# Performance work log

Hardware: AMD Instinct MI355X
Metric: run time of the kernel (lower is better)

Reference implementation:

```python
import jax, jax.numpy as jnp
import numpy as np

L = 3          # num_layer
E_DIM = 64     # emb_dim
B = 4          # graphs per batch
N = 20000      # nodes per graph
E = 320000     # edges per graph
IN_DIM = 21    # raw node feature dim (Linear(21, emb_dim))
BN_EPS = 1e-5


def setup_inputs() -> dict:
    key = jax.random.key(0)
    ks = jax.random.split(key, 16)
    h2 = 2 * E_DIM
    inp = {
        "x": jax.random.normal(ks[0], (B, N, IN_DIM), dtype=jnp.float32),
        "edge_index": jax.random.randint(ks[1], (B, 2, E), 0, N, dtype=jnp.int64),
        "edge_attr": jax.random.normal(ks[2], (B, E, 1), dtype=jnp.float32),
        # layer-0 input node embedding Linear(21, emb)
        "inW": jax.random.normal(ks[3], (IN_DIM, E_DIM), dtype=jnp.float32) * 0.1,
        "inb": jnp.zeros((E_DIM,), dtype=jnp.float32),
        # per-layer edge encoder Linear(1, emb)
        "edgeW": jax.random.normal(ks[4], (L, 1, E_DIM), dtype=jnp.float32) * 0.1,
        "edgeb": jnp.zeros((L, E_DIM), dtype=jnp.float32),
        # per-layer MLP: Linear(2e,2e) -> BN(2e) -> ReLU -> Linear(2e,e)
        "W1": jax.random.normal(ks[5], (L, h2, h2), dtype=jnp.float32) * 0.05,
        "b1": jnp.zeros((L, h2), dtype=jnp.float32),
        "gamma": jnp.ones((L, h2), dtype=jnp.float32),
        "beta": jnp.zeros((L, h2), dtype=jnp.float32),
        "W2": jax.random.normal(ks[6], (L, h2, E_DIM), dtype=jnp.float32) * 0.05,
        "b2": jnp.zeros((L, E_DIM), dtype=jnp.float32),
    }
    return inp


def _batchnorm_train(h, g, b):
    # BatchNorm1d in training mode: per-graph stats over the node dim, biased var
    m = h.mean(axis=0)
    v = jnp.mean((h - m) ** 2, axis=0)
    return (h - m) * jax.lax.rsqrt(v + BN_EPS) * g + b


def _gin_layer(xg, eig, eag, W1l, b1l, gl, bel, W2l, b2l):
    # xg [N,e], eig [2,E], eag [E,e]
    x_j = xg[eig[0]]                                   # gather source nodes [E,e]
    msg = jnp.concatenate([x_j, eag], axis=-1)         # [E,2e]
    aggr = jax.ops.segment_sum(msg, eig[1], num_segments=N)  # scatter-add [N,2e]
    h = aggr @ W1l + b1l
    h = _batchnorm_train(h, gl, bel)
    h = jax.nn.relu(h)
    return h @ W2l + b2l                               # [N,e]


def reference(x, edge_index, edge_attr, inW, inb, edgeW, edgeb, W1, b1, gamma, beta, W2, b2):
    h = x
    for l in range(L):
        ea = edge_attr @ edgeW[l] + edgeb[l]           # [B,E,e] edge embeddings
        if l == 0:
            h = h @ inW + inb                          # [B,N,e]
        h = jax.vmap(_gin_layer, in_axes=(0, 0, 0, None, None, None, None, None, None))(
            h, edge_index, ea, W1[l], b1[l], gamma[l], beta[l], W2[l], b2[l])
        if l < L - 1:                                  # drop_ratio=0 -> dropout is identity
            h = jax.nn.relu(h)
    return h  # JK='last'
```

## Files before the change

kernel.cpp:

```cpp
#include <hip/hip_runtime.h>
#include <hip/hip_bf16.h>
#include <hip/hip_fp16.h>

#define NB 4
#define NN 20000
#define NE 320000
#define IND 21
#define ED 64
#define H2 128
#define CAP 48
#define RNODES 2500
#define ECHUNK 2560
#define BN_EPS 1e-5f

typedef __attribute__((ext_vector_type(8))) short bf16x8;
typedef __attribute__((ext_vector_type(4))) float f32x4;

__device__ __forceinline__ short f2bf(float f) {
    unsigned u = __float_as_uint(f);
    u += 0x7fffu + ((u >> 16) & 1u);
    return (short)(u >> 16);
}


__global__ __launch_bounds__(256) void k_fill_direct(
    const int* __restrict__ ei, const float* __restrict__ eattr,
    int* __restrict__ cnt, unsigned int* __restrict__ bucket)
{
    const int b = blockIdx.y;
    const int range = blockIdx.x & 7;
    const int chunk = blockIdx.x >> 3;
    const int lo = range * RNODES, hi = lo + RNODES;
    const int* srcp = ei + (size_t)b * 2 * NE;
    const int* dstp = srcp + NE;
    const float* ap = eattr + (size_t)b * NE;
    #pragma unroll
    for (int it = 0; it < ECHUNK / 256; ++it) {
        const int e = chunk * ECHUNK + it * 256 + threadIdx.x;
        const int dst = dstp[e];
        if (dst >= lo && dst < hi) {
            const int src = srcp[e];
            const float a = ap[e];
            const int node = b * NN + dst;
            const int p = atomicAdd(&cnt[node], 1);
            if (p < CAP)
                bucket[(size_t)node * CAP + p] =
                    ((unsigned int)src & 0xffffu) | (__float_as_uint(a) & 0xffff0000u);
        }
    }
}

__global__ __launch_bounds__(256) void k_in(
    const float* __restrict__ x, const float* __restrict__ inW,
    const float* __restrict__ inb, __half* __restrict__ h)
{
    const int b = blockIdx.y;
    const int t = blockIdx.x * 256 + threadIdx.x;
    const int n = t >> 6;
    const int c = t & 63;
    if (n >= NN) return;
    const float* xr = x + ((size_t)b * NN + n) * IND;
    float acc = inb[c];
    #pragma unroll
    for (int k = 0; k < IND; ++k) acc += xr[k] * inW[k * ED + c];
    h[((size_t)b * NN + n) * ED + c] = __float2half(acc);
}

__global__ __launch_bounds__(256) void k_prep(
    const float* __restrict__ W1, const float* __restrict__ W2,
    const float* __restrict__ edgeW, const float* __restrict__ edgeb,
    short* __restrict__ W1T, short* __restrict__ W2T,
    float* __restrict__ uv_all, float* __restrict__ stats_all)
{
    const int l = blockIdx.x;
    const int tid = threadIdx.x;
    ((float4*)(stats_all + l * 1024))[tid] = make_float4(0.f, 0.f, 0.f, 0.f);
    for (int i = tid; i < H2 * ED; i += 256) {
        const int j = i >> 6, k = i & 63;
        W1T[l * 8192 + i] = f2bf(W1[(size_t)l * H2 * H2 + k * H2 + j]);
    }
    for (int i = tid; i < ED * H2; i += 256) {
        const int c = i >> 7, k = i & 127;
        W2T[l * 8192 + i] = f2bf(W2[(size_t)l * H2 * ED + k * ED + c]);
    }
    if (tid < H2) {
        float u = 0.f, v = 0.f;
        for (int k = 0; k < ED; ++k) {
            const float w = W1[(size_t)l * H2 * H2 + (ED + k) * H2 + tid];
            u += edgeW[l * ED + k] * w;
            v += edgeb[l * ED + k] * w;
        }
        uv_all[l * 256 + tid] = u;
        uv_all[l * 256 + H2 + tid] = v;
    }
}


__global__ __launch_bounds__(256) void k_aggr_stats(
    const __half* __restrict__ h, const unsigned int* __restrict__ bucket,
    const int* __restrict__ cnt_arr, const short* __restrict__ W1Tl,
    const float* __restrict__ b1l, const float* __restrict__ uv_l,
    short* __restrict__ aggr_bf, float* __restrict__ s_attr,
    float* __restrict__ stats_l, int write_sattr)
{
    __shared__ short w1t[H2 * 72];
    __shared__ short atb[16 * 72];
    __shared__ float sdl[16], ddl[16];
    __shared__ float uL[H2], vL[H2], bbL[H2];
    const int tid = threadIdx.x;
    const int g = blockIdx.x & 7;
    const int b = g >> 1;
    const int t = ((int)blockIdx.x >> 3) * 2 + (g & 1);
    const int n0 = t * 16;

    for (int i = tid; i < 1024; i += 256)
        *(uint4*)&w1t[(i >> 3) * 72 + (i & 7) * 8] = ((const uint4*)W1Tl)[i];
    if (tid < H2) { uL[tid] = uv_l[tid]; vL[tid] = uv_l[H2 + tid]; bbL[tid] = b1l[tid]; }

    {
        const int node = n0 + (tid >> 4);
        const int q = tid & 15;
        const int cntraw = cnt_arr[b * NN + node];
        const int cnt = min(cntraw, CAP);
        const unsigned int* row = bucket + (size_t)(b * NN + node) * CAP;
        const __half* hp = h + (size_t)b * NN * ED + q * 4;
        float4 a0 = make_float4(0.f, 0.f, 0.f, 0.f);
        float4 a1 = make_float4(0.f, 0.f, 0.f, 0.f);
        float sa = 0.f;
        int j = 0;
        for (; j + 4 <= cnt; j += 4) {
            const uint4 ss = *(const uint4*)(row + j);
            const uint2 r0 = *(const uint2*)(hp + (size_t)(ss.x & 0xffffu) * ED);
            const uint2 r1 = *(const uint2*)(hp + (size_t)(ss.y & 0xffffu) * ED);
            const uint2 r2 = *(const uint2*)(hp + (size_t)(ss.z & 0xffffu) * ED);
            const uint2 r3 = *(const uint2*)(hp + (size_t)(ss.w & 0xffffu) * ED);
            sa += __uint_as_float(ss.x & 0xffff0000u) + __uint_as_float(ss.y & 0xffff0000u)
                + __uint_as_float(ss.z & 0xffff0000u) + __uint_as_float(ss.w & 0xffff0000u);
            const float2 f0a = __half22float2(*(const __half2*)&r0.x);
            const float2 f0b = __half22float2(*(const __half2*)&r0.y);
            const float2 f1a = __half22float2(*(const __half2*)&r1.x);
            const float2 f1b = __half22float2(*(const __half2*)&r1.y);
            const float2 f2a = __half22float2(*(const __half2*)&r2.x);
            const float2 f2b = __half22float2(*(const __half2*)&r2.y);
            const float2 f3a = __half22float2(*(const __half2*)&r3.x);
            const float2 f3b = __half22float2(*(const __half2*)&r3.y);
            a0.x += f0a.x + f1a.x; a0.y += f0a.y + f1a.y;
            a0.z += f0b.x + f1b.x; a0.w += f0b.y + f1b.y;
            a1.x += f2a.x + f3a.x; a1.y += f2a.y + f3a.y;
            a1.z += f2b.x + f3b.x; a1.w += f2b.y + f3b.y;
        }
        for (; j < cnt; ++j) {
            const unsigned e = row[j];
            sa += __uint_as_float(e & 0xffff0000u);
            const uint2 r0 = *(const uint2*)(hp + (size_t)(e & 0xffffu) * ED);
            const float2 fa = __half22float2(*(const __half2*)&r0.x);
            const float2 fb = __half22float2(*(const __half2*)&r0.y);
            a0.x += fa.x; a0.y += fa.y; a0.z += fb.x; a0.w += fb.y;
        }
        a0.x += a1.x; a0.y += a1.y; a0.z += a1.z; a0.w += a1.w;
        uint2 pk;
        pk.x = (unsigned short)f2bf(a0.x) | ((unsigned int)(unsigned short)f2bf(a0.y) << 16);
        pk.y = (unsigned short)f2bf(a0.z) | ((unsigned int)(unsigned short)f2bf(a0.w) << 16);
        *(uint2*)&atb[(tid >> 4) * 72 + q * 4] = pk;
        *(uint2*)&aggr_bf[((size_t)b * NN + node) * ED + q * 4] = pk;
        if (q == 0) {
            sdl[tid >> 4] = sa;
            ddl[tid >> 4] = (float)cntraw;
            if (write_sattr) s_attr[b * NN + node] = sa;
        }
    }
    __syncthreads();

    const int l = tid & 63;
    const int w = tid >> 6;
    const int m = l & 15, quad = l >> 4;
    f32x4 acc0 = {0.f, 0.f, 0.f, 0.f}, acc1 = {0.f, 0.f, 0.f, 0.f};
    #pragma unroll
    for (int kc = 0; kc < 2; ++kc) {
        const bf16x8 fa = *(const bf16x8*)&atb[m * 72 + kc * 32 + quad * 8];
        const bf16x8 fb0 = *(const bf16x8*)&w1t[((w * 2 + 0) * 16 + m) * 72 + kc * 32 + quad * 8];
        const bf16x8 fb1 = *(const bf16x8*)&w1t[((w * 2 + 1) * 16 + m) * 72 + kc * 32 + quad * 8];
        acc0 = __builtin_amdgcn_mfma_f32_16x16x32_bf16(fa, fb0, acc0, 0, 0, 0);
        acc1 = __builtin_amdgcn_mfma_f32_16x16x32_bf16(fa, fb1, acc1, 0, 0, 0);
    }
    float sa_r[4], dg_r[4];
    #pragma unroll
    for (int r = 0; r < 4; ++r) { sa_r[r] = sdl[quad * 4 + r]; dg_r[r] = ddl[quad * 4 + r]; }
    #pragma unroll
    for (int t2 = 0; t2 < 2; ++t2) {
        const int j = (w * 2 + t2) * 16 + m;
        const float u = uL[j], v = vL[j], bb = bbL[j];
        float ls = 0.f, lq = 0.f;
        #pragma unroll
        for (int r = 0; r < 4; ++r) {
            const float h1 = (t2 ? acc1[r] : acc0[r]) + sa_r[r] * u + dg_r[r] * v + bb;
            ls += h1; lq += h1 * h1;
        }
        ls += __shfl_xor(ls, 16); ls += __shfl_xor(ls, 32);
        lq += __shfl_xor(lq, 16); lq += __shfl_xor(lq, 32);
        if (l < 16) {
            atomicAdd(&stats_l[b * H2 + j], ls);
            atomicAdd(&stats_l[NB * H2 + b * H2 + j], lq);
        }
    }
}

__global__ __launch_bounds__(256) void k_mlp_out(
    const short* __restrict__ aggr_bf, const float* __restrict__ s_attr,
    const int* __restrict__ cnt_arr, const short* __restrict__ W1Tl,
    const short* __restrict__ W2Tl, const float* __restrict__ b1l,
    const float* __restrict__ uv_l, const float* __restrict__ stats_l,
    const float* __restrict__ gamma_l, const float* __restrict__ beta_l,
    const float* __restrict__ b2l, __half* __restrict__ outh,
    float* __restrict__ outf, int last)
{
    __shared__ short wt[H2 * 72];
    __shared__ short ab[32 * 72];
    __shared__ short pb[32 * 136];
    __shared__ float sdl[32], ddl[32];
    __shared__ float uL[H2], vL[H2], bbL[H2], scL[H2], shL[H2];
    const int tid = threadIdx.x;
    const int g = blockIdx.x & 7;
    const int b = g >> 1;
    const int t = ((int)blockIdx.x >> 3) * 2 + (g & 1);
    if (t >= NN / 32) return;
    const int n0 = t * 32;

    for (int i = tid; i < 1024; i += 256)
        *(uint4*)&wt[(i >> 3) * 72 + (i & 7) * 8] = ((const uint4*)W1Tl)[i];
    *(uint4*)&ab[(tid >> 3) * 72 + (tid & 7) * 8] =
        ((const uint4*)(aggr_bf + ((size_t)b * NN + n0) * ED))[tid];
    if (tid < 32) sdl[tid] = s_attr[b * NN + n0 + tid];
    else if (tid < 64) ddl[tid - 32] = (float)cnt_arr[b * NN + n0 + tid - 32];
    if (tid < H2) {
        const int j = tid;
        const float mm = stats_l[b * H2 + j] * (1.f / NN);
        const float var = fmaxf(stats_l[NB * H2 + b * H2 + j] * (1.f / NN) - mm * mm, 0.f);
        const float rs = rsqrtf(var + BN_EPS);
        const float sc = gamma_l[j] * rs;
        scL[j] = sc;
        shL[j] = beta_l[j] - mm * sc;
        uL[j] = uv_l[j]; vL[j] = uv_l[H2 + j]; bbL[j] = b1l[j];
    }
    __syncthreads();

    const int l = tid & 63;
    const int w = tid >> 6;
    const int m = l & 15, quad = l >> 4;
    const int mt = w & 1;
    {
        const int jb = (w >> 1) * 4;
        f32x4 acc[4];
        #pragma unroll
        for (int i = 0; i < 4; ++i) acc[i] = (f32x4){0.f, 0.f, 0.f, 0.f};
        #pragma unroll
        for (int kc = 0; kc < 2; ++kc) {
            const bf16x8 fa = *(const bf16x8*)&ab[(mt * 16 + m) * 72 + kc * 32 + quad * 8];
            #pragma unroll
            for (int t2 = 0; t2 < 4; ++t2) {
                const bf16x8 fb = *(const bf16x8*)&wt[((jb + t2) * 16 + m) * 72 + kc * 32 + quad * 8];
                acc[t2] = __builtin_amdgcn_mfma_f32_16x16x32_bf16(fa, fb, acc[t2], 0, 0, 0);
            }
        }
        float sa_r[4], dg_r[4];
        #pragma unroll
        for (int r = 0; r < 4; ++r) {
            const int row = mt * 16 + quad * 4 + r;
            sa_r[r] = sdl[row]; dg_r[r] = ddl[row];
        }
        #pragma unroll
        for (int t2 = 0; t2 < 4; ++t2) {
            const int j = (jb + t2) * 16 + m;
            const float u = uL[j], v = vL[j], bb = bbL[j];
            const float sc = scL[j], sh = shL[j];
            #pragma unroll
            for (int r = 0; r < 4; ++r) {
                const float h1 = acc[t2][r] + sa_r[r] * u + dg_r[r] * v + bb;
                pb[(mt * 16 + quad * 4 + r) * 136 + j] = f2bf(fmaxf(h1 * sc + sh, 0.f));
            }
        }
    }
    __syncthreads();
    for (int i = tid; i < 1024; i += 256)
        *(uint4*)&wt[(i >> 4) * 136 + (i & 15) * 8] = ((const uint4*)W2Tl)[i];
    __syncthreads();
    {
        const int nb = (w >> 1) * 2;
        f32x4 acc2[2];
        acc2[0] = (f32x4){0.f, 0.f, 0.f, 0.f};
        acc2[1] = (f32x4){0.f, 0.f, 0.f, 0.f};
        #pragma unroll
        for (int kc = 0; kc < 4; ++kc) {
            const bf16x8 fa = *(const bf16x8*)&pb[(mt * 16 + m) * 136 + kc * 32 + quad * 8];
            #pragma unroll
            for (int t2 = 0; t2 < 2; ++t2) {
                const bf16x8 fb = *(const bf16x8*)&wt[((nb + t2) * 16 + m) * 136 + kc * 32 + quad * 8];
                acc2[t2] = __builtin_amdgcn_mfma_f32_16x16x32_bf16(fa, fb, acc2[t2], 0, 0, 0);
            }
        }
        #pragma unroll
        for (int t2 = 0; t2 < 2; ++t2) {
            const int c = (nb + t2) * 16 + m;
            const float bb2 = b2l[c];
            #pragma unroll
            for (int r = 0; r < 4; ++r) {
                const int row = mt * 16 + quad * 4 + r;
                const size_t idx = ((size_t)b * NN + n0 + row) * ED + c;
                float o = acc2[t2][r] + bb2;
                if (last) outf[idx] = o;
                else outh[idx] = __float2half(fmaxf(o, 0.f));
            }
        }
    }
}


extern "C" void kernel_launch(void* const* d_in, const int* in_sizes, int n_in,
                              void* d_out, int out_size, void* d_ws, size_t ws_size,
                              hipStream_t stream) {
    const float* x     = (const float*)d_in[0];
    const int*   ei    = (const int*)d_in[1];
    const float* eattr = (const float*)d_in[2];
    const float* inW   = (const float*)d_in[3];
    const float* inb   = (const float*)d_in[4];
    const float* edgeW = (const float*)d_in[5];
    const float* edgeb = (const float*)d_in[6];
    const float* W1    = (const float*)d_in[7];
    const float* b1    = (const float*)d_in[8];
    const float* gamma = (const float*)d_in[9];
    const float* beta  = (const float*)d_in[10];
    const float* W2    = (const float*)d_in[11];
    const float* b2    = (const float*)d_in[12];
    float* out = (float*)d_out;

    float* s_attr = (float*)d_ws;
    int*   cnt    = (int*)(s_attr + NB * NN);
    unsigned int* bucket = (unsigned int*)(cnt + NB * NN);
    short* aggr_bf = (short*)(bucket + (size_t)NB * NN * CAP);
    __half* hh    = (__half*)(aggr_bf + (size_t)NB * NN * ED);
    short* W1T    = (short*)(hh + (size_t)NB * NN * ED);
    short* W2T    = W1T + 3 * 8192;
    float* uv_all = (float*)(W2T + 3 * 8192);
    float* stats  = uv_all + 3 * 256;

    hipMemsetAsync(cnt, 0, (size_t)NB * NN * sizeof(int), stream);

    const dim3 eg((NE / ECHUNK) * 8, NB);
    k_fill_direct<<<eg, 256, 0, stream>>>(ei, eattr, cnt, bucket);
    k_in<<<dim3(NN * ED / 256, NB), 256, 0, stream>>>(x, inW, inb, hh);
    k_prep<<<3, 256, 0, stream>>>(W1, W2, edgeW, edgeb, W1T, W2T, uv_all, stats);

    const int nblk1 = NB * (NN / 16);
    const int nblk2 = ((NN / 32 + 1) / 2) * 16;
    for (int l = 0; l < 3; ++l) {
        k_aggr_stats<<<nblk1, 256, 0, stream>>>(hh, bucket, cnt,
            W1T + l * 8192, b1 + l * H2, uv_all + l * 256,
            aggr_bf, s_attr, stats + l * 1024, (l == 0) ? 1 : 0);
        k_mlp_out<<<nblk2, 256, 0, stream>>>(aggr_bf, s_attr, cnt,
            W1T + l * 8192, W2T + l * 8192, b1 + l * H2, uv_all + l * 256,
            stats + l * 1024, gamma + l * H2, beta + l * H2, b2 + l * ED,
            hh, out, (l == 2) ? 1 : 0);
    }
}
```

Before: 386.1 us.

## Two-pass edge bucketing and larger node tiles in aggregation and MLP kernels

The direct bucket fill, which had each of 8 node ranges rescan every edge, is replaced by two passes. A compaction pass bins edges by destination range into staging buffers using shared-memory atomics, then a scatter pass fills the per-node buckets. The aggregation kernel now handles 32 nodes per block with 16-byte gathers (8 halves per thread) and 4 MFMA tiles per wave. The MLP kernel handles 64 nodes per block with a bounds check on the ragged last tile. This cuts redundant edge reads and raises per-block work and load width, at the cost of an extra launch and a staging buffer. Staging capacity is fixed, so a skewed edge distribution could overflow it.

```diff
diff --git a/kernel.cpp b/kernel.cpp
--- a/kernel.cpp
+++ b/kernel.cpp
@@ -10,7 +10,7 @@
 #define H2 128
 #define CAP 48
 #define RNODES 2500
-#define ECHUNK 2560
+#define SCAP 45056
 #define BN_EPS 1e-5f
 
 typedef __attribute__((ext_vector_type(8))) short bf16x8;
@@ -22,30 +22,72 @@
     return (short)(u >> 16);
 }
 
-
-__global__ __launch_bounds__(256) void k_fill_direct(
+__device__ __forceinline__ void add8(float* ac, const uint4 rv) {
+    const float2 f0 = __half22float2(*(const __half2*)&rv.x);
+    const float2 f1 = __half22float2(*(const __half2*)&rv.y);
+    const float2 f2 = __half22float2(*(const __half2*)&rv.z);
+    const float2 f3 = __half22float2(*(const __half2*)&rv.w);
+    ac[0] += f0.x; ac[1] += f0.y; ac[2] += f1.x; ac[3] += f1.y;
+    ac[4] += f2.x; ac[5] += f2.y; ac[6] += f3.x; ac[7] += f3.y;
+}
+
+
+__global__ __launch_bounds__(256) void k_compact(
     const int* __restrict__ ei, const float* __restrict__ eattr,
-    int* __restrict__ cnt, unsigned int* __restrict__ bucket)
-{
+    uint2* __restrict__ stage, int* __restrict__ rcnt)
+{
+    __shared__ uint2 bins[8][384];
+    __shared__ int lcnt[8];
+    __shared__ int lbase[8];
     const int b = blockIdx.y;
-    const int range = blockIdx.x & 7;
-    const int chunk = blockIdx.x >> 3;
-    const int lo = range * RNODES, hi = lo + RNODES;
+    const int e0 = blockIdx.x * 2048;
+    const int tid = threadIdx.x;
+    if (tid < 8) lcnt[tid] = 0;
+    __syncthreads();
     const int* srcp = ei + (size_t)b * 2 * NE;
     const int* dstp = srcp + NE;
     const float* ap = eattr + (size_t)b * NE;
     #pragma unroll
-    for (int it = 0; it < ECHUNK / 256; ++it) {
-        const int e = chunk * ECHUNK + it * 256 + threadIdx.x;
-        const int dst = dstp[e];
-        if (dst >= lo && dst < hi) {
+    for (int it = 0; it < 8; ++it) {
+        const int e = e0 + it * 256 + tid;
+        if (e < NE) {
+            const int dst = dstp[e];
             const int src = srcp[e];
             const float a = ap[e];
-            const int node = b * NN + dst;
+            const int r = dst / RNODES;
+            const unsigned lo = ((unsigned)src & 0xffffu) | (__float_as_uint(a) & 0xffff0000u);
+            const int p = atomicAdd(&lcnt[r], 1);
+            if (p < 384) bins[r][p] = make_uint2(lo, (unsigned)dst);
+        }
+    }
+    __syncthreads();
+    if (tid < 8) lbase[tid] = atomicAdd(&rcnt[b * 8 + tid], min(lcnt[tid], 384));
+    __syncthreads();
+    for (int r = 0; r < 8; ++r) {
+        const int c = min(lcnt[r], 384);
+        uint2* dstg = stage + (size_t)(b * 8 + r) * SCAP + lbase[r];
+        for (int i = tid; i < c; i += 256) dstg[i] = bins[r][i];
+    }
+}
+
+__global__ __launch_bounds__(256) void k_scatter(
+    const uint2* __restrict__ stage, const int* __restrict__ rcnt,
+    int* __restrict__ cnt, unsigned int* __restrict__ bucket)
+{
+    const int r = blockIdx.x & 7;
+    const int q = blockIdx.x >> 3;
+    const int b = q & 3;
+    const int slice = q >> 2;
+    const int count = rcnt[b * 8 + r];
+    const uint2* st = stage + (size_t)(b * 8 + r) * SCAP;
+    #pragma unroll
+    for (int it = 0; it < 16; ++it) {
+        const int idx = slice * 4096 + it * 256 + threadIdx.x;
+        if (idx < count) {
+            const uint2 rec = st[idx];
+            const int node = b * NN + (int)rec.y;
             const int p = atomicAdd(&cnt[node], 1);
-            if (p < CAP)
-                bucket[(size_t)node * CAP + p] =
-                    ((unsigned int)src & 0xffffu) | (__float_as_uint(a) & 0xffff0000u);
+            if (p < CAP) bucket[(size_t)node * CAP + p] = rec.x;
         }
     }
 }
@@ -104,68 +146,58 @@
     float* __restrict__ stats_l, int write_sattr)
 {
     __shared__ short w1t[H2 * 72];
-    __shared__ short atb[16 * 72];
-    __shared__ float sdl[16], ddl[16];
+    __shared__ short atb[32 * 72];
+    __shared__ float sdl[32], ddl[32];
     __shared__ float uL[H2], vL[H2], bbL[H2];
     const int tid = threadIdx.x;
     const int g = blockIdx.x & 7;
     const int b = g >> 1;
     const int t = ((int)blockIdx.x >> 3) * 2 + (g & 1);
-    const int n0 = t * 16;
+    if (t >= NN / 32) return;
+    const int n0 = t * 32;
 
     for (int i = tid; i < 1024; i += 256)
         *(uint4*)&w1t[(i >> 3) * 72 + (i & 7) * 8] = ((const uint4*)W1Tl)[i];
     if (tid < H2) { uL[tid] = uv_l[tid]; vL[tid] = uv_l[H2 + tid]; bbL[tid] = b1l[tid]; }
 
     {
-        const int node = n0 + (tid >> 4);
-        const int q = tid & 15;
+        const int node = n0 + (tid >> 3);
+        const int q = tid & 7;
         const int cntraw = cnt_arr[b * NN + node];
         const int cnt = min(cntraw, CAP);
         const unsigned int* row = bucket + (size_t)(b * NN + node) * CAP;
-        const __half* hp = h + (size_t)b * NN * ED + q * 4;
-        float4 a0 = make_float4(0.f, 0.f, 0.f, 0.f);
-        float4 a1 = make_float4(0.f, 0.f, 0.f, 0.f);
+        const __half* hp = h + (size_t)b * NN * ED + q * 8;
+        float ac[8];
+        #pragma unroll
+        for (int i = 0; i < 8; ++i) ac[i] = 0.f;
         float sa = 0.f;
         int j = 0;
         for (; j + 4 <= cnt; j += 4) {
             const uint4 ss = *(const uint4*)(row + j);
-            const uint2 r0 = *(const uint2*)(hp + (size_t)(ss.x & 0xffffu) * ED);
-            const uint2 r1 = *(const uint2*)(hp + (size_t)(ss.y & 0xffffu) * ED);
-            const uint2 r2 = *(const uint2*)(hp + (size_t)(ss.z & 0xffffu) * ED);
-            const uint2 r3 = *(const uint2*)(hp + (size_t)(ss.w & 0xffffu) * ED);
+            const uint4 r0 = *(const uint4*)(hp + (size_t)(ss.x & 0xffffu) * ED);
+            const uint4 r1 = *(const uint4*)(hp + (size_t)(ss.y & 0xffffu) * ED);
+            const uint4 r2 = *(const uint4*)(hp + (size_t)(ss.z & 0xffffu) * ED);
+            const uint4 r3 = *(const uint4*)(hp + (size_t)(ss.w & 0xffffu) * ED);
             sa += __uint_as_float(ss.x & 0xffff0000u) + __uint_as_float(ss.y & 0xffff0000u)
                 + __uint_as_float(ss.z & 0xffff0000u) + __uint_as_float(ss.w & 0xffff0000u);
-            const float2 f0a = __half22float2(*(const __half2*)&r0.x);
-            const float2 f0b = __half22float2(*(const __half2*)&r0.y);
-            const float2 f1a = __half22float2(*(const __half2*)&r1.x);
-            const float2 f1b = __half22float2(*(const __half2*)&r1.y);
-            const float2 f2a = __half22float2(*(const __half2*)&r2.x);
-            const float2 f2b = __half22float2(*(const __half2*)&r2.y);
-            const float2 f3a = __half22float2(*(const __half2*)&r3.x);
-            const float2 f3b = __half22float2(*(const __half2*)&r3.y);
-            a0.x += f0a.x + f1a.x; a0.y += f0a.y + f1a.y;
-            a0.z += f0b.x + f1b.x; a0.w += f0b.y + f1b.y;
-            a1.x += f2a.x + f3a.x; a1.y += f2a.y + f3a.y;
-            a1.z += f2b.x + f3b.x; a1.w += f2b.y + f3b.y;
+            add8(ac, r0); add8(ac, r1); add8(ac, r2); add8(ac, r3);
         }
         for (; j < cnt; ++j) {
             const unsigned e = row[j];
             sa += __uint_as_float(e & 0xffff0000u);
-            const uint2 r0 = *(const uint2*)(hp + (size_t)(e & 0xffffu) * ED);
-            const float2 fa = __half22float2(*(const __half2*)&r0.x);
-            const float2 fb = __half22float2(*(const __half2*)&r0.y);
-            a0.x += fa.x; a0.y += fa.y; a0.z += fb.x; a0.w += fb.y;
-        }
-        a0.x += a1.x; a0.y += a1.y; a0.z += a1.z; a0.w += a1.w;
-        uint2 pk;
-        pk.x = (unsigned short)f2bf(a0.x) | ((unsigned int)(unsigned short)f2bf(a0.y) << 16);
-        pk.y = (unsigned short)f2bf(a0.z) | ((unsigned int)(unsigned short)f2bf(a0.w) << 16);
-        *(uint2*)&atb[(tid >> 4) * 72 + q * 4] = pk;
-        *(uint2*)&aggr_bf[((size_t)b * NN + node) * ED + q * 4] = pk;
+            const uint4 r0 = *(const uint4*)(hp + (size_t)(e & 0xffffu) * ED);
+            add8(ac, r0);
+        }
+        uint4 pk;
+        pk.x = (unsigned short)f2bf(ac[0]) | ((unsigned int)(unsigned short)f2bf(ac[1]) << 16);
+        pk.y = (unsigned short)f2bf(ac[2]) | ((unsigned int)(unsigned short)f2bf(ac[3]) << 16);
+        pk.z = (unsigned short)f2bf(ac[4]) | ((unsigned int)(unsigned short)f2bf(ac[5]) << 16);
+        pk.w = (unsigned short)f2bf(ac[6]) | ((unsigned int)(unsigned short)f2bf(ac[7]) << 16);
+        *(uint4*)&atb[(tid >> 3) * 72 + q * 8] = pk;
+        *(uint4*)&aggr_bf[((size_t)b * NN + node) * ED + q * 8] = pk;
         if (q == 0) {
-            sdl[tid >> 4] = sa;
-            ddl[tid >> 4] = (float)cntraw;
+            sdl[tid >> 3] = sa;
+            ddl[tid >> 3] = (float)cntraw;
             if (write_sattr) s_attr[b * NN + node] = sa;
         }
     }
@@ -174,26 +206,34 @@
     const int l = tid & 63;
     const int w = tid >> 6;
     const int m = l & 15, quad = l >> 4;
-    f32x4 acc0 = {0.f, 0.f, 0.f, 0.f}, acc1 = {0.f, 0.f, 0.f, 0.f};
+    const int mt = w & 1;
+    const int jb = (w >> 1) * 4;
+    f32x4 acc[4];
+    #pragma unroll
+    for (int i = 0; i < 4; ++i) acc[i] = (f32x4){0.f, 0.f, 0.f, 0.f};
     #pragma unroll
     for (int kc = 0; kc < 2; ++kc) {
-        const bf16x8 fa = *(const bf16x8*)&atb[m * 72 + kc * 32 + quad * 8];
-        const bf16x8 fb0 = *(const bf16x8*)&w1t[((w * 2 + 0) * 16 + m) * 72 + kc * 32 + quad * 8];
-        const bf16x8 fb1 = *(const bf16x8*)&w1t[((w * 2 + 1) * 16 + m) * 72 + kc * 32 + quad * 8];
-        acc0 = __builtin_amdgcn_mfma_f32_16x16x32_bf16(fa, fb0, acc0, 0, 0, 0);
-        acc1 = __builtin_amdgcn_mfma_f32_16x16x32_bf16(fa, fb1, acc1, 0, 0, 0);
+        const bf16x8 fa = *(const bf16x8*)&atb[(mt * 16 + m) * 72 + kc * 32 + quad * 8];
+        #pragma unroll
+        for (int t2 = 0; t2 < 4; ++t2) {
+            const bf16x8 fb = *(const bf16x8*)&w1t[((jb + t2) * 16 + m) * 72 + kc * 32 + quad * 8];
+            acc[t2] = __builtin_amdgcn_mfma_f32_16x16x32_bf16(fa, fb, acc[t2], 0, 0, 0);
+        }
     }
     float sa_r[4], dg_r[4];
     #pragma unroll
-    for (int r = 0; r < 4; ++r) { sa_r[r] = sdl[quad * 4 + r]; dg_r[r] = ddl[quad * 4 + r]; }
-    #pragma unroll
-    for (int t2 = 0; t2 < 2; ++t2) {
-        const int j = (w * 2 + t2) * 16 + m;
+    for (int r = 0; r < 4; ++r) {
+        const int row = mt * 16 + quad * 4 + r;
+        sa_r[r] = sdl[row]; dg_r[r] = ddl[row];
+    }
+    #pragma unroll
+    for (int t2 = 0; t2 < 4; ++t2) {
+        const int j = (jb + t2) * 16 + m;
         const float u = uL[j], v = vL[j], bb = bbL[j];
         float ls = 0.f, lq = 0.f;
         #pragma unroll
         for (int r = 0; r < 4; ++r) {
-            const float h1 = (t2 ? acc1[r] : acc0[r]) + sa_r[r] * u + dg_r[r] * v + bb;
+            const float h1 = acc[t2][r] + sa_r[r] * u + dg_r[r] * v + bb;
             ls += h1; lq += h1 * h1;
         }
         ls += __shfl_xor(ls, 16); ls += __shfl_xor(ls, 32);
@@ -215,23 +255,24 @@
     float* __restrict__ outf, int last)
 {
     __shared__ short wt[H2 * 72];
-    __shared__ short ab[32 * 72];
-    __shared__ short pb[32 * 136];
-    __shared__ float sdl[32], ddl[32];
+    __shared__ short ab[64 * 72];
+    __shared__ short pb[64 * 136];
+    __shared__ float sdl[64], ddl[64];
     __shared__ float uL[H2], vL[H2], bbL[H2], scL[H2], shL[H2];
     const int tid = threadIdx.x;
     const int g = blockIdx.x & 7;
     const int b = g >> 1;
     const int t = ((int)blockIdx.x >> 3) * 2 + (g & 1);
-    if (t >= NN / 32) return;
-    const int n0 = t * 32;
+    if (t >= (NN + 63) / 64) return;
+    const int n0 = t * 64;
 
     for (int i = tid; i < 1024; i += 256)
         *(uint4*)&wt[(i >> 3) * 72 + (i & 7) * 8] = ((const uint4*)W1Tl)[i];
-    *(uint4*)&ab[(tid >> 3) * 72 + (tid & 7) * 8] =
-        ((const uint4*)(aggr_bf + ((size_t)b * NN + n0) * ED))[tid];
-    if (tid < 32) sdl[tid] = s_attr[b * NN + n0 + tid];
-    else if (tid < 64) ddl[tid - 32] = (float)cnt_arr[b * NN + n0 + tid - 32];
+    for (int i = tid; i < 512; i += 256)
+        *(uint4*)&ab[(i >> 3) * 72 + (i & 7) * 8] =
+            ((const uint4*)(aggr_bf + ((size_t)b * NN + n0) * ED))[i];
+    if (tid < 64) sdl[tid] = s_attr[b * NN + n0 + tid];
+    else if (tid < 128) ddl[tid - 64] = (float)cnt_arr[b * NN + n0 + tid - 64];
     if (tid < H2) {
         const int j = tid;
         const float mm = stats_l[b * H2 + j] * (1.f / NN);
@@ -247,36 +288,34 @@
     const int l = tid & 63;
     const int w = tid >> 6;
     const int m = l & 15, quad = l >> 4;
-    const int mt = w & 1;
     {
-        const int jb = (w >> 1) * 4;
-        f32x4 acc[4];
-        #pragma unroll
-        for (int i = 0; i < 4; ++i) acc[i] = (f32x4){0.f, 0.f, 0.f, 0.f};
+        f32x4 acc[8];
+        #pragma unroll
+        for (int i = 0; i < 8; ++i) acc[i] = (f32x4){0.f, 0.f, 0.f, 0.f};
         #pragma unroll
         for (int kc = 0; kc < 2; ++kc) {
-            const bf16x8 fa = *(const bf16x8*)&ab[(mt * 16 + m) * 72 + kc * 32 + quad * 8];
+            const bf16x8 fa = *(const bf16x8*)&ab[(w * 16 + m) * 72 + kc * 32 + quad * 8];
             #pragma unroll
-            for (int t2 = 0; t2 < 4; ++t2) {
-                const bf16x8 fb = *(const bf16x8*)&wt[((jb + t2) * 16 + m) * 72 + kc * 32 + quad * 8];
+            for (int t2 = 0; t2 < 8; ++t2) {
+                const bf16x8 fb = *(const bf16x8*)&wt[(t2 * 16 + m) * 72 + kc * 32 + quad * 8];
                 acc[t2] = __builtin_amdgcn_mfma_f32_16x16x32_bf16(fa, fb, acc[t2], 0, 0, 0);
             }
         }
         float sa_r[4], dg_r[4];
         #pragma unroll
         for (int r = 0; r < 4; ++r) {
-            const int row = mt * 16 + quad * 4 + r;
+            const int row = w * 16 + quad * 4 + r;
             sa_r[r] = sdl[row]; dg_r[r] = ddl[row];
         }
         #pragma unroll
-        for (int t2 = 0; t2 < 4; ++t2) {
-            const int j = (jb + t2) * 16 + m;
+        for (int t2 = 0; t2 < 8; ++t2) {
+            const int j = t2 * 16 + m;
             const float u = uL[j], v = vL[j], bb = bbL[j];
             const float sc = scL[j], sh = shL[j];
             #pragma unroll
             for (int r = 0; r < 4; ++r) {
                 const float h1 = acc[t2][r] + sa_r[r] * u + dg_r[r] * v + bb;
-                pb[(mt * 16 + quad * 4 + r) * 136 + j] = f2bf(fmaxf(h1 * sc + sh, 0.f));
+                pb[(w * 16 + quad * 4 + r) * 136 + j] = f2bf(fmaxf(h1 * sc + sh, 0.f));
             }
         }
     }
@@ -285,30 +324,32 @@
         *(uint4*)&wt[(i >> 4) * 136 + (i & 15) * 8] = ((const uint4*)W2Tl)[i];
     __syncthreads();
     {
-        const int nb = (w >> 1) * 2;
-        f32x4 acc2[2];
-        acc2[0] = (f32x4){0.f, 0.f, 0.f, 0.f};
-        acc2[1] = (f32x4){0.f, 0.f, 0.f, 0.f};
+        f32x4 acc2[4];
+        #pragma unroll
+        for (int i = 0; i < 4; ++i) acc2[i] = (f32x4){0.f, 0.f, 0.f, 0.f};
         #pragma unroll
         for (int kc = 0; kc < 4; ++kc) {
-            const bf16x8 fa = *(const bf16x8*)&pb[(mt * 16 + m) * 136 + kc * 32 + quad * 8];
+            const bf16x8 fa = *(const bf16x8*)&pb[(w * 16 + m) * 136 + kc * 32 + quad * 8];
             #pragma unroll
-            for (int t2 = 0; t2 < 2; ++t2) {
-                const bf16x8 fb = *(const bf16x8*)&wt[((nb + t2) * 16 + m) * 136 + kc * 32 + quad * 8];
+            for (int t2 = 0; t2 < 4; ++t2) {
+                const bf16x8 fb = *(const bf16x8*)&wt[(t2 * 16 + m) * 136 + kc * 32 + quad * 8];
                 acc2[t2] = __builtin_amdgcn_mfma_f32_16x16x32_bf16(fa, fb, acc2[t2], 0, 0, 0);
             }
         }
         #pragma unroll
-        for (int t2 = 0; t2 < 2; ++t2) {
-            const int c = (nb + t2) * 16 + m;
+        for (int t2 = 0; t2 < 4; ++t2) {
+            const int c = t2 * 16 + m;
             const float bb2 = b2l[c];
             #pragma unroll
             for (int r = 0; r < 4; ++r) {
-                const int row = mt * 16 + quad * 4 + r;
-                const size_t idx = ((size_t)b * NN + n0 + row) * ED + c;
-                float o = acc2[t2][r] + bb2;
-                if (last) outf[idx] = o;
-                else outh[idx] = __float2half(fmaxf(o, 0.f));
+                const int row = w * 16 + quad * 4 + r;
+                const int n = n0 + row;
+                if (n < NN) {
+                    const size_t idx = ((size_t)b * NN + n) * ED + c;
+                    float o = acc2[t2][r] + bb2;
+                    if (last) outf[idx] = o;
+                    else outh[idx] = __float2half(fmaxf(o, 0.f));
+                }
             }
         }
     }
@@ -335,7 +376,9 @@
 
     float* s_attr = (float*)d_ws;
     int*   cnt    = (int*)(s_attr + NB * NN);
-    unsigned int* bucket = (unsigned int*)(cnt + NB * NN);
+    int*   rcnt   = cnt + NB * NN;
+    uint2* stage  = (uint2*)(rcnt + 64);
+    unsigned int* bucket = (unsigned int*)(stage + (size_t)32 * SCAP);
     short* aggr_bf = (short*)(bucket + (size_t)NB * NN * CAP);
     __half* hh    = (__half*)(aggr_bf + (size_t)NB * NN * ED);
     short* W1T    = (short*)(hh + (size_t)NB * NN * ED);
@@ -343,15 +386,15 @@
     float* uv_all = (float*)(W2T + 3 * 8192);
     float* stats  = uv_all + 3 * 256;
 
-    hipMemsetAsync(cnt, 0, (size_t)NB * NN * sizeof(int), stream);
-
-    const dim3 eg((NE / ECHUNK) * 8, NB);
-    k_fill_direct<<<eg, 256, 0, stream>>>(ei, eattr, cnt, bucket);
+    hipMemsetAsync(cnt, 0, ((size_t)NB * NN + 64) * sizeof(int), stream);
+
+    k_compact<<<dim3((NE + 2047) / 2048, NB), 256, 0, stream>>>(ei, eattr, stage, rcnt);
+    k_scatter<<<8 * 44, 256, 0, stream>>>(stage, rcnt, cnt, bucket);
     k_in<<<dim3(NN * ED / 256, NB), 256, 0, stream>>>(x, inW, inb, hh);
     k_prep<<<3, 256, 0, stream>>>(W1, W2, edgeW, edgeb, W1T, W2T, uv_all, stats);
 
-    const int nblk1 = NB * (NN / 16);
-    const int nblk2 = ((NN / 32 + 1) / 2) * 16;
+    const int nblk1 = 8 * ((NN / 32 + 1) / 2);
+    const int nblk2 = 8 * (((NN + 63) / 64 + 1) / 2);
     for (int l = 0; l < 3; ++l) {
         k_aggr_stats<<<nblk1, 256, 0, stream>>>(hh, bucket, cnt,
             W1T + l * 8192, b1 + l * H2, uv_all + l * 256,
```

Result: no change. 388.7 us (+0.7%).
